# Kernel tuning notes

Measured on AMD Instinct MI355X. Metric: run time of the kernel, lower is better.

The kernel has to match this reference:

```python
import jax, jax.numpy as jnp
import numpy as np

N_NODES = 40000

def setup_inputs() -> dict:
    key = jax.random.key(0)
    k1, k2, k3, k4 = jax.random.split(key, 4)
    x = jax.random.normal(k1, (N_NODES, 256), dtype=jnp.float32)
    edge_index = jax.random.randint(k2, (2, 640000), 0, N_NODES, dtype=jnp.int64)
    W = jax.random.normal(k3, (256, 128), dtype=jnp.float32) * (1.0 / np.sqrt(256))
    b = jax.random.normal(k4, (128,), dtype=jnp.float32) * 0.01
    return {"x": x, "edge_index": edge_index, "W": W, "b": b}

def reference(x, edge_index, W, b):
    N = x.shape[0]
    # GCNConv: add self-loops, symmetric degree normalization, linear, aggregate, bias
    loops = jnp.arange(N, dtype=edge_index.dtype)
    src = jnp.concatenate([edge_index[0], loops])  # message sources j
    dst = jnp.concatenate([edge_index[1], loops])  # targets i
    ones = jnp.ones_like(dst, dtype=x.dtype)
    deg = jax.ops.segment_sum(ones, dst, num_segments=N)  # in-degree incl. self-loop
    dinv = jnp.where(deg > 0, jax.lax.rsqrt(deg), 0.0)
    norm = dinv[src] * dinv[dst]  # [E+N]
    xw = x @ W  # transform first (in_dim -> out_dim), as in PyG GCNConv
    msgs = norm[:, None] * xw[src]  # [E+N, out_dim]
    agg = jax.ops.segment_sum(msgs, dst, num_segments=N) + b
    return jax.nn.relu(agg)  # dropout_value == 0 -> no dropout
```

## Files before the change

### kernel.cpp

```cpp
#include <hip/hip_runtime.h>

#define N_NODES 40000
#define IN_DIM 256
#define OUT_DIM 128
#define CAP 64
#define GEMM_BLOCKS 625
#define EPT 8
#define FILL_BLOCKS ((640000 + 256 * EPT - 1) / (256 * EPT))

typedef __bf16 bf16x8 __attribute__((ext_vector_type(8)));
typedef float floatx4 __attribute__((ext_vector_type(4)));

__device__ __forceinline__ int clamp_idx(int v) {
    unsigned u = (unsigned)v;
    return (u < (unsigned)N_NODES) ? v : 0;
}

__device__ __forceinline__ int get_idx(const void* p, long long i, int is64) {
    if (is64) return clamp_idx((int)((const long long*)p)[i]);
    return clamp_idx(((const int*)p)[i]);
}

__device__ __forceinline__ float bflo(unsigned u) {
    union { unsigned i; float f; } c; c.i = u << 16; return c.f;
}
__device__ __forceinline__ float bfhi(unsigned u) {
    union { unsigned i; float f; } c; c.i = u & 0xFFFF0000u; return c.f;
}

__global__ void prep_r14(const int* __restrict__ edge32, int* __restrict__ flag,
                         int* __restrict__ cnt, const float* __restrict__ W,
                         __bf16* __restrict__ wswz) {
    int i = blockIdx.x * 256 + threadIdx.x;
    if (i < N_NODES) cnt[i] = 0;
    if (i < IN_DIM * OUT_DIM) {
        int j    = i & 7;
        int lane = (i >> 3) & 63;
        int tile = i >> 9;
        int ct = tile & 7, kc = tile >> 3;
        int k = kc * 32 + (lane >> 4) * 8 + j;
        int n = ct * 16 + (lane & 15);
        wswz[i] = (__bf16)W[k * OUT_DIM + n];
    }
    if (blockIdx.x == 0) {
        __shared__ int sh[256];
        int t = threadIdx.x;
        int nz = 0;
        for (int k = t; k < 1000; k += 256) nz |= (edge32[2 * k + 1] != 0);
        sh[t] = nz;
        __syncthreads();
        for (int off = 128; off > 0; off >>= 1) {
            if (t < off) sh[t] |= sh[t + off];
            __syncthreads();
        }
        if (t == 0) *flag = sh[0] ? 0 : 1;
    }
}

__global__ __launch_bounds__(256) void main_r14(
    const float* __restrict__ x, const __bf16* __restrict__ wswz,
    __bf16* __restrict__ xwb,
    const void* __restrict__ edge, int E, const int* __restrict__ flag,
    int* __restrict__ cnt, unsigned short* __restrict__ bucket) {
    int t = threadIdx.x;
    if (blockIdx.x < GEMM_BLOCKS) {
        int wave = t >> 6, lane = t & 63;
        int quad = lane >> 4, m16 = lane & 15;
        int m = blockIdx.x * 64 + wave * 16 + m16;
        const float* xrow = x + (long long)m * IN_DIM;
        const bf16x8* wp = (const bf16x8*)wswz;

        floatx4 acc[8];
#pragma unroll
        for (int ct = 0; ct < 8; ++ct) acc[ct] = (floatx4){0.f, 0.f, 0.f, 0.f};

#pragma unroll
        for (int kc = 0; kc < 8; ++kc) {
            int k0 = kc * 32 + quad * 8;
            float4 xa = *(const float4*)(xrow + k0);
            float4 xb = *(const float4*)(xrow + k0 + 4);
            bf16x8 af;
            af[0] = (__bf16)xa.x; af[1] = (__bf16)xa.y;
            af[2] = (__bf16)xa.z; af[3] = (__bf16)xa.w;
            af[4] = (__bf16)xb.x; af[5] = (__bf16)xb.y;
            af[6] = (__bf16)xb.z; af[7] = (__bf16)xb.w;
#pragma unroll
            for (int ct = 0; ct < 8; ++ct) {
                bf16x8 bf = wp[(kc * 8 + ct) * 64 + lane];
                acc[ct] = __builtin_amdgcn_mfma_f32_16x16x32_bf16(af, bf, acc[ct], 0, 0, 0);
            }
        }

        int rbase = blockIdx.x * 64 + wave * 16 + quad * 4;
#pragma unroll
        for (int ct = 0; ct < 8; ++ct) {
            int col = ct * 16 + m16;
#pragma unroll
            for (int r = 0; r < 4; ++r)
                xwb[(long long)(rbase + r) * OUT_DIM + col] = (__bf16)acc[ct][r];
        }
    } else {
        int is64 = *flag;
        int base = (blockIdx.x - GEMM_BLOCKS) * (256 * EPT) + t * EPT;
        int s[EPT], d[EPT], p[EPT];
#pragma unroll
        for (int q = 0; q < EPT; ++q) {
            int e = base + q;
            s[q] = (e < E) ? get_idx(edge, e, is64) : 0;
            d[q] = (e < E) ? get_idx(edge, (long long)E + e, is64) : 0;
        }
#pragma unroll
        for (int q = 0; q < EPT; ++q)
            p[q] = (base + q < E) ? atomicAdd(&cnt[d[q]], 1) : CAP;
#pragma unroll
        for (int q = 0; q < EPT; ++q)
            if (p[q] < CAP) bucket[d[q] * CAP + p[q]] = (unsigned short)s[q];
    }
}

__global__ void gather_r14(const unsigned short* __restrict__ bucket,
                           const int* __restrict__ cnt,
                           const unsigned* __restrict__ xwd, const float* __restrict__ b,
                           float* __restrict__ out) {
    int node = blockIdx.x * 4 + (threadIdx.x >> 6);
    int lane = threadIdx.x & 63;
    if (node >= N_NODES) return;
    float b0 = b[2 * lane], b1 = b[2 * lane + 1];
    int cn_true = cnt[node];
    int take = cn_true < CAP ? cn_true : CAP;
    float dd = rsqrtf((float)(cn_true + 1));
    unsigned us = xwd[node * 64 + lane];
    float a0 = dd * dd * bflo(us);
    float a1 = dd * dd * bfhi(us);

    int s_l = 0; float nrm_l = 0.0f;
    if (lane < take) {
        s_l = (int)bucket[node * CAP + lane];
        nrm_l = dd * rsqrtf((float)(cnt[s_l] + 1));
    }
    int j = 0;
    for (; j + 16 <= take; j += 16) {
        unsigned uu[16]; float nn[16];
#pragma unroll
        for (int q = 0; q < 16; ++q) {
            int s = __shfl(s_l, j + q);
            nn[q] = __shfl(nrm_l, j + q);
            uu[q] = xwd[s * 64 + lane];
        }
#pragma unroll
        for (int q = 0; q < 16; ++q) {
            a0 += nn[q] * bflo(uu[q]);
            a1 += nn[q] * bfhi(uu[q]);
        }
    }
    for (; j + 8 <= take; j += 8) {
        unsigned uu[8]; float nn[8];
#pragma unroll
        for (int q = 0; q < 8; ++q) {
            int s = __shfl(s_l, j + q);
            nn[q] = __shfl(nrm_l, j + q);
            uu[q] = xwd[s * 64 + lane];
        }
#pragma unroll
        for (int q = 0; q < 8; ++q) {
            a0 += nn[q] * bflo(uu[q]);
            a1 += nn[q] * bfhi(uu[q]);
        }
    }
    for (; j < take; ++j) {
        int   s = __shfl(s_l, j);
        float n = __shfl(nrm_l, j);
        unsigned u = xwd[s * 64 + lane];
        a0 += n * bflo(u); a1 += n * bfhi(u);
    }
    float2 r;
    r.x = fmaxf(a0 + b0, 0.0f);
    r.y = fmaxf(a1 + b1, 0.0f);
    *(float2*)&out[node * OUT_DIM + 2 * lane] = r;
}

extern "C" void kernel_launch(void* const* d_in, const int* in_sizes, int n_in,
                              void* d_out, int out_size, void* d_ws, size_t ws_size,
                              hipStream_t stream) {
    const float* x   = (const float*)d_in[0];
    const void* edge = d_in[1];
    const float* W   = (const float*)d_in[2];
    const float* b   = (const float*)d_in[3];
    float* out       = (float*)d_out;

    int E = in_sizes[1] / 2;

    char* ws = (char*)d_ws;
    int*            cnt    = (int*)(ws);
    int*            flag   = (int*)(ws + 160000);
    __bf16*         wswz   = (__bf16*)(ws + 160256);
    unsigned short* bucket = (unsigned short*)(ws + 225792);
    __bf16*         xwb    = (__bf16*)(ws + 5345792);

    int fill_blocks = (E + 256 * EPT - 1) / (256 * EPT);
    prep_r14<<<160, 256, 0, stream>>>((const int*)edge, flag, cnt, W, wswz);
    main_r14<<<GEMM_BLOCKS + fill_blocks, 256, 0, stream>>>(
        x, wswz, xwb, edge, E, flag, cnt, bucket);
    gather_r14<<<N_NODES / 4, 256, 0, stream>>>(bucket, cnt, (const unsigned*)xwb, b, out);
}
```

Baseline: 154.8 us.

## Partition bucket fill by XCC-local destination ranges with work-stealing chunk queues

```diff
diff --git a/kernel.cpp b/kernel.cpp
--- a/kernel.cpp
+++ b/kernel.cpp
@@ -5,8 +5,9 @@
 #define OUT_DIM 128
 #define CAP 64
 #define GEMM_BLOCKS 625
-#define EPT 8
-#define FILL_BLOCKS ((640000 + 256 * EPT - 1) / (256 * EPT))
+#define FILL_BLOCKS 625
+#define RANGE_SZ 5000
+#define CHUNK 8192
 
 typedef __bf16 bf16x8 __attribute__((ext_vector_type(8)));
 typedef float floatx4 __attribute__((ext_vector_type(4)));
@@ -28,11 +29,12 @@
     union { unsigned i; float f; } c; c.i = u & 0xFFFF0000u; return c.f;
 }
 
-__global__ void prep_r14(const int* __restrict__ edge32, int* __restrict__ flag,
-                         int* __restrict__ cnt, const float* __restrict__ W,
-                         __bf16* __restrict__ wswz) {
+__global__ void prep_r17(const int* __restrict__ edge32, int* __restrict__ flag,
+                         int* __restrict__ cnt, int* __restrict__ qhead,
+                         const float* __restrict__ W, __bf16* __restrict__ wswz) {
     int i = blockIdx.x * 256 + threadIdx.x;
     if (i < N_NODES) cnt[i] = 0;
+    if (i < 8) qhead[i * 16] = 0;
     if (i < IN_DIM * OUT_DIM) {
         int j    = i & 7;
         int lane = (i >> 3) & 63;
@@ -57,11 +59,12 @@
     }
 }
 
-__global__ __launch_bounds__(256) void main_r14(
+__global__ __launch_bounds__(256) void main_r17(
     const float* __restrict__ x, const __bf16* __restrict__ wswz,
     __bf16* __restrict__ xwb,
     const void* __restrict__ edge, int E, const int* __restrict__ flag,
-    int* __restrict__ cnt, unsigned short* __restrict__ bucket) {
+    int* __restrict__ cnt, int* __restrict__ qhead,
+    unsigned short* __restrict__ bucket) {
     int t = threadIdx.x;
     if (blockIdx.x < GEMM_BLOCKS) {
         int wave = t >> 6, lane = t & 63;
@@ -100,25 +103,32 @@
                 xwb[(long long)(rbase + r) * OUT_DIM + col] = (__bf16)acc[ct][r];
         }
     } else {
+        int xcc;
+        asm("s_getreg_b32 %0, hwreg(HW_REG_XCC_ID)" : "=s"(xcc));
+        xcc &= 7;
         int is64 = *flag;
-        int base = (blockIdx.x - GEMM_BLOCKS) * (256 * EPT) + t * EPT;
-        int s[EPT], d[EPT], p[EPT];
-#pragma unroll
-        for (int q = 0; q < EPT; ++q) {
-            int e = base + q;
-            s[q] = (e < E) ? get_idx(edge, e, is64) : 0;
-            d[q] = (e < E) ? get_idx(edge, (long long)E + e, is64) : 0;
-        }
-#pragma unroll
-        for (int q = 0; q < EPT; ++q)
-            p[q] = (base + q < E) ? atomicAdd(&cnt[d[q]], 1) : CAP;
-#pragma unroll
-        for (int q = 0; q < EPT; ++q)
-            if (p[q] < CAP) bucket[d[q] * CAP + p[q]] = (unsigned short)s[q];
-    }
-}
-
-__global__ void gather_r14(const unsigned short* __restrict__ bucket,
+        int lo = xcc * RANGE_SZ;
+        __shared__ int sh_c;
+        for (;;) {
+            if (t == 0) sh_c = atomicAdd(&qhead[xcc * 16], CHUNK);
+            __syncthreads();
+            int c = sh_c;
+            if (c >= E) break;
+            int cend = c + CHUNK; if (cend > E) cend = E;
+            for (int e = c + t; e < cend; e += 256) {
+                int d = get_idx(edge, (long long)E + e, is64);
+                if ((unsigned)(d - lo) < (unsigned)RANGE_SZ) {
+                    int s = get_idx(edge, e, is64);
+                    int pos = atomicAdd(&cnt[d], 1);
+                    if (pos < CAP) bucket[d * CAP + pos] = (unsigned short)s;
+                }
+            }
+            __syncthreads();
+        }
+    }
+}
+
+__global__ void gather_r17(const unsigned short* __restrict__ bucket,
                            const int* __restrict__ cnt,
                            const unsigned* __restrict__ xwd, const float* __restrict__ b,
                            float* __restrict__ out) {
@@ -139,20 +149,6 @@
         nrm_l = dd * rsqrtf((float)(cnt[s_l] + 1));
     }
     int j = 0;
-    for (; j + 16 <= take; j += 16) {
-        unsigned uu[16]; float nn[16];
-#pragma unroll
-        for (int q = 0; q < 16; ++q) {
-            int s = __shfl(s_l, j + q);
-            nn[q] = __shfl(nrm_l, j + q);
-            uu[q] = xwd[s * 64 + lane];
-        }
-#pragma unroll
-        for (int q = 0; q < 16; ++q) {
-            a0 += nn[q] * bflo(uu[q]);
-            a1 += nn[q] * bfhi(uu[q]);
-        }
-    }
     for (; j + 8 <= take; j += 8) {
         unsigned uu[8]; float nn[8];
 #pragma unroll
@@ -192,14 +188,14 @@
 
     char* ws = (char*)d_ws;
     int*            cnt    = (int*)(ws);
-    int*            flag   = (int*)(ws + 160000);
-    __bf16*         wswz   = (__bf16*)(ws + 160256);
-    unsigned short* bucket = (unsigned short*)(ws + 225792);
-    __bf16*         xwb    = (__bf16*)(ws + 5345792);
-
-    int fill_blocks = (E + 256 * EPT - 1) / (256 * EPT);
-    prep_r14<<<160, 256, 0, stream>>>((const int*)edge, flag, cnt, W, wswz);
-    main_r14<<<GEMM_BLOCKS + fill_blocks, 256, 0, stream>>>(
-        x, wswz, xwb, edge, E, flag, cnt, bucket);
-    gather_r14<<<N_NODES / 4, 256, 0, stream>>>(bucket, cnt, (const unsigned*)xwb, b, out);
-}
+    int*            qhead  = (int*)(ws + 160000);
+    int*            flag   = (int*)(ws + 160512);
+    __bf16*         wswz   = (__bf16*)(ws + 160576);
+    unsigned short* bucket = (unsigned short*)(ws + 226112);
+    __bf16*         xwb    = (__bf16*)(ws + 5346112);
+
+    prep_r17<<<160, 256, 0, stream>>>((const int*)edge, flag, cnt, qhead, W, wswz);
+    main_r17<<<GEMM_BLOCKS + FILL_BLOCKS, 256, 0, stream>>>(
+        x, wswz, xwb, edge, E, flag, cnt, qhead, bucket);
+    gather_r17<<<N_NODES / 4, 256, 0, stream>>>(bucket, cnt, (const unsigned*)xwb, b, out);
+}
```

After: 170.8 us. 10.4% more time.
